# Kernel tuning notes

Hardware: AMD Instinct MI355X
Metric: run time of the kernel (lower is better)

The kernel has to match this reference:

```python
import jax, jax.numpy as jnp
import numpy as np

N_NODES = 50000
N_EDGES = 800000
IN_FEATS = 128
OUT_FEATS = 256
EPS = 1e-5


def _layer_norm(x, g, b):
    mu = jnp.mean(x, axis=-1, keepdims=True)
    var = jnp.var(x, axis=-1, keepdims=True)
    return (x - mu) * jax.lax.rsqrt(var + EPS) * g + b


def setup_inputs() -> dict:
    key = jax.random.key(0)
    ks = jax.random.split(key, 6)
    h = jax.random.normal(ks[0], (N_NODES, IN_FEATS), dtype=jnp.float32)
    src = jax.random.randint(ks[1], (N_EDGES,), 0, N_NODES, dtype=jnp.int32)
    dst = jax.random.randint(ks[2], (N_EDGES,), 0, N_NODES, dtype=jnp.int32)
    s_in = 1.0 / np.sqrt(IN_FEATS)
    s_out = 1.0 / np.sqrt(OUT_FEATS)
    return {
        "h": h,
        "src": src,
        "dst": dst,
        "ln1_g": jnp.ones((IN_FEATS,), jnp.float32),
        "ln1_b": jnp.zeros((IN_FEATS,), jnp.float32),
        "W_self": jax.random.normal(ks[3], (IN_FEATS, OUT_FEATS), jnp.float32) * s_in,
        "W_neigh": jax.random.normal(ks[4], (IN_FEATS, OUT_FEATS), jnp.float32) * s_in,
        "b_neigh": jnp.zeros((OUT_FEATS,), jnp.float32),
        "ln2_g": jnp.ones((OUT_FEATS,), jnp.float32),
        "ln2_b": jnp.zeros((OUT_FEATS,), jnp.float32),
        "W_si": jax.random.normal(ks[5], (OUT_FEATS, OUT_FEATS), jnp.float32) * s_out,
        "b_si": jnp.zeros((OUT_FEATS,), jnp.float32),
    }


def reference(h, src, dst, ln1_g, ln1_b, W_self, W_neigh, b_neigh, ln2_g, ln2_b, W_si, b_si):
    # Pre-norm
    h = _layer_norm(h, ln1_g, ln1_b)
    h_skip = h
    # SAGEConv 'mean': gather src features, segment-mean over dst
    msg = h[src]  # [E, in_feats]
    agg = jax.ops.segment_sum(msg, dst, num_segments=N_NODES)  # [N, in_feats]
    deg = jax.ops.segment_sum(jnp.ones((src.shape[0],), h.dtype), dst, num_segments=N_NODES)
    mean_neigh = agg / jnp.maximum(deg, 1.0)[:, None]
    conv = h @ W_self + mean_neigh @ W_neigh + b_neigh  # [N, out_feats]
    # dropout is identity in eval mode
    # residual skip with channel repeat (out_feat_factor = 2)
    conv = conv + jnp.repeat(h_skip, OUT_FEATS // IN_FEATS, axis=-1)
    # self-interaction: norm -> Linear -> ELU -> residual
    x = _layer_norm(conv, ln2_g, ln2_b)
    out = jax.nn.elu(x @ W_si + b_si) + x
    return out
```

## Files before the change

kernel.cpp:

```cpp
#include <hip/hip_runtime.h>
#include <math.h>

#define N_NODES 50000
#define N_EDGES 800000
#define IN_F 128
#define OUT_F 256
#define EPS 1e-5f
#define BM 16
#define NSCAN 196

typedef __attribute__((ext_vector_type(8))) short short8;
typedef __attribute__((ext_vector_type(4))) float f32x4;

__device__ inline float wave_reduce_sum(float v) {
    #pragma unroll
    for (int m = 32; m >= 1; m >>= 1) v += __shfl_xor(v, m, 64);
    return v;
}

__device__ inline unsigned short f2bf(float f) {
    unsigned int x = __float_as_uint(f);
    return (unsigned short)((x + 0x7fffu + ((x >> 16) & 1u)) >> 16);
}
__device__ inline float bf2f(unsigned short u) {
    return __uint_as_float((unsigned int)u << 16);
}
__device__ inline void split2(float v, unsigned short& hi, unsigned short& lo) {
    hi = f2bf(v);
    lo = f2bf(v - bf2f(hi));
}

__global__ __launch_bounds__(256) void ln1_kernel(const float* __restrict__ h,
        const float* __restrict__ g, const float* __restrict__ b,
        float* __restrict__ hln) {
    int wave = threadIdx.x >> 6;
    int lane = threadIdx.x & 63;
    int row = blockIdx.x * 4 + wave;
    if (row >= N_NODES) return;
    float2 v = ((const float2*)(h + (size_t)row * IN_F))[lane];
    float s  = wave_reduce_sum(v.x + v.y);
    float sq = wave_reduce_sum(v.x * v.x + v.y * v.y);
    float mu = s * (1.0f / IN_F);
    float var = sq * (1.0f / IN_F) - mu * mu;
    float rs = rsqrtf(var + EPS);
    float2 gv = ((const float2*)g)[lane];
    float2 bv = ((const float2*)b)[lane];
    float2 o;
    o.x = (v.x - mu) * rs * gv.x + bv.x;
    o.y = (v.y - mu) * rs * gv.y + bv.y;
    ((float2*)(hln + (size_t)row * IN_F))[lane] = o;
}

__global__ __launch_bounds__(256) void prep_kernel(const float* __restrict__ Wself,
        const float* __restrict__ Wneigh, const float* __restrict__ Wsi,
        unsigned int* __restrict__ W2Th, unsigned int* __restrict__ W2Tl,
        unsigned int* __restrict__ WsiTh, unsigned int* __restrict__ WsiTl) {
    __shared__ float tile[64][65];
    int bx = blockIdx.x;
    int mat = bx >> 4;
    int tr = ((bx >> 2) & 3) * 64;
    int tc = (bx & 3) * 64;
    int t = threadIdx.x;
    int c = t & 63, r0 = t >> 6;
    for (int i = 0; i < 16; ++i) {
        int k = tr + r0 + i * 4;
        float v;
        if (mat == 0) v = (k < 128) ? Wself[(size_t)k * 256 + tc + c]
                                    : Wneigh[(size_t)(k - 128) * 256 + tc + c];
        else          v = Wsi[(size_t)k * 256 + tc + c];
        tile[r0 + i * 4][c] = v;
    }
    __syncthreads();
    unsigned int* oh = (mat == 0) ? W2Th : WsiTh;
    unsigned int* ol = (mat == 0) ? W2Tl : WsiTl;
    int c2 = t & 31, rr = t >> 5;
    for (int i = 0; i < 8; ++i) {
        int n = rr + i * 8;
        float a = tile[c2 * 2][n];
        float b = tile[c2 * 2 + 1][n];
        unsigned short ah, al, bh, bl;
        split2(a, ah, al);
        split2(b, bh, bl);
        size_t idx = (size_t)(tc + n) * 128 + (tr >> 1) + c2;
        oh[idx] = (unsigned int)ah | ((unsigned int)bh << 16);
        ol[idx] = (unsigned int)al | ((unsigned int)bl << 16);
    }
}

__global__ __launch_bounds__(256) void hist_kernel(const int* __restrict__ dst,
                                                   int* __restrict__ cnt) {
    int e = blockIdx.x * 256 + threadIdx.x;
    if (e < N_EDGES) atomicAdd(&cnt[dst[e]], 1);
}

__global__ __launch_bounds__(256) void scan1_kernel(const int* __restrict__ cnt,
        int* __restrict__ curs, int* __restrict__ bsum) {
    int t = threadIdx.x;
    int i = blockIdx.x * 256 + t;
    int v = (i < N_NODES) ? cnt[i] : 0;
    int x = v;
    #pragma unroll
    for (int off = 1; off < 64; off <<= 1) {
        int y = __shfl_up(x, off, 64);
        if ((t & 63) >= off) x += y;
    }
    __shared__ int wsum[4];
    if ((t & 63) == 63) wsum[t >> 6] = x;
    __syncthreads();
    int wofs = 0;
    for (int w = 0; w < (t >> 6); ++w) wofs += wsum[w];
    int incl = x + wofs;
    if (i < N_NODES) curs[i] = incl - v;
    if (t == 255) bsum[blockIdx.x] = incl;
}

__global__ __launch_bounds__(256) void scan2_kernel(int* __restrict__ bsum) {
    int t = threadIdx.x;
    int v = (t < NSCAN) ? bsum[t] : 0;
    int x = v;
    #pragma unroll
    for (int off = 1; off < 64; off <<= 1) {
        int y = __shfl_up(x, off, 64);
        if ((t & 63) >= off) x += y;
    }
    __shared__ int wsum[4];
    if ((t & 63) == 63) wsum[t >> 6] = x;
    __syncthreads();
    int wofs = 0;
    for (int w = 0; w < (t >> 6); ++w) wofs += wsum[w];
    if (t < NSCAN) bsum[t] = x + wofs - v;
}

__global__ __launch_bounds__(256) void scan3_kernel(int* __restrict__ curs,
        const int* __restrict__ bsum) {
    int i = blockIdx.x * 256 + threadIdx.x;
    if (i < N_NODES) curs[i] += bsum[blockIdx.x];
}

__global__ __launch_bounds__(256) void fill_kernel(const int* __restrict__ src,
        const int* __restrict__ dst, int* __restrict__ curs, int* __restrict__ eidx) {
    int e = blockIdx.x * 256 + threadIdx.x;
    if (e >= N_EDGES) return;
    int d = dst[e];
    int pos = atomicAdd(&curs[d], 1);
    eidx[pos] = src[e];
}

__global__ __launch_bounds__(256) void gather_kernel(const float* __restrict__ hln,
        const int* __restrict__ cnt, const int* __restrict__ curs,
        const int* __restrict__ eidx, float* __restrict__ mean) {
    int wave = threadIdx.x >> 6;
    int lane = threadIdx.x & 63;
    int row = blockIdx.x * 4 + wave;
    if (row >= N_NODES) return;
    int deg = cnt[row];
    int end = curs[row];
    int start = end - deg;
    float2 acc = make_float2(0.f, 0.f);
    for (int j0 = 0; j0 < deg; j0 += 64) {
        int mye = (j0 + lane < deg) ? eidx[start + j0 + lane] : 0;
        int m = min(64, deg - j0);
        for (int jj = 0; jj < m; ++jj) {
            int s = __shfl(mye, jj, 64);
            float2 v = ((const float2*)(hln + (size_t)s * IN_F))[lane];
            acc.x += v.x;
            acc.y += v.y;
        }
    }
    float scale = 1.0f / fmaxf((float)deg, 1.0f);
    float2 o; o.x = acc.x * scale; o.y = acc.y * scale;
    ((float2*)(mean + (size_t)row * IN_F))[lane] = o;
}

__global__ __launch_bounds__(256) void fused_kernel(
        const float* __restrict__ hlnf, const float* __restrict__ meanf,
        const unsigned short* __restrict__ W2Th, const unsigned short* __restrict__ W2Tl,
        const unsigned short* __restrict__ WsiTh, const unsigned short* __restrict__ WsiTl,
        const float* __restrict__ bneigh, const float* __restrict__ ln2g,
        const float* __restrict__ ln2b, const float* __restrict__ bsi,
        float* __restrict__ out) {
    __shared__ float sAf[BM][264];
    __shared__ unsigned short sAh[BM][264];
    __shared__ unsigned short sAl[BM][264];
    __shared__ float sC[BM][260];
    __shared__ float spart[4][BM][2];

    const int t = threadIdx.x;
    const int lane = t & 63;
    const int wave = t >> 6;
    const int lrow = lane & 15;
    const int lk = (lane >> 4) * 8;
    const int base = blockIdx.x * BM;

    for (int i = t; i < BM * 64; i += 256) {
        int r = i >> 6, ch = i & 63;
        int node = base + r;
        float4 v = (ch < 32) ? ((const float4*)(hlnf + (size_t)node * IN_F))[ch]
                             : ((const float4*)(meanf + (size_t)node * IN_F))[ch - 32];
        int cb = (ch < 32) ? ch * 4 : 128 + (ch - 32) * 4;
        *(float4*)&sAf[r][cb] = v;
        unsigned short h0, l0, h1, l1, h2, l2, h3, l3;
        split2(v.x, h0, l0); split2(v.y, h1, l1);
        split2(v.z, h2, l2); split2(v.w, h3, l3);
        uint2 ph, pl;
        ph.x = (unsigned int)h0 | ((unsigned int)h1 << 16);
        ph.y = (unsigned int)h2 | ((unsigned int)h3 << 16);
        pl.x = (unsigned int)l0 | ((unsigned int)l1 << 16);
        pl.y = (unsigned int)l2 | ((unsigned int)l3 << 16);
        *(uint2*)&sAh[r][cb] = ph;
        *(uint2*)&sAl[r][cb] = pl;
    }
    __syncthreads();

    f32x4 am[4];
    #pragma unroll
    for (int cf = 0; cf < 4; ++cf) am[cf] = (f32x4)(0.f);
    #pragma unroll
    for (int k0 = 0; k0 < 256; k0 += 32) {
        short8 ah = *(const short8*)&sAh[lrow][k0 + lk];
        short8 al = *(const short8*)&sAl[lrow][k0 + lk];
        #pragma unroll
        for (int cf = 0; cf < 4; ++cf) {
            int col = wave * 64 + cf * 16 + lrow;
            short8 bh = *(const short8*)(W2Th + (size_t)col * 256 + k0 + lk);
            short8 bl = *(const short8*)(W2Tl + (size_t)col * 256 + k0 + lk);
            am[cf] = __builtin_amdgcn_mfma_f32_16x16x32_bf16(ah, bh, am[cf], 0, 0, 0);
            am[cf] = __builtin_amdgcn_mfma_f32_16x16x32_bf16(al, bh, am[cf], 0, 0, 0);
            am[cf] = __builtin_amdgcn_mfma_f32_16x16x32_bf16(ah, bl, am[cf], 0, 0, 0);
        }
    }

    #pragma unroll
    for (int cf = 0; cf < 4; ++cf) {
        int col = wave * 64 + cf * 16 + lrow;
        float bn = bneigh[col];
        #pragma unroll
        for (int q = 0; q < 4; ++q) {
            int row = (lane >> 4) * 4 + q;
            sC[row][col] = am[cf][q] + bn + sAf[row][col >> 1];
        }
    }
    __syncthreads();

    float cv[BM];
    {
        #pragma unroll
        for (int r = 0; r < BM; ++r) {
            float c = sC[r][t];
            cv[r] = c;
            float s  = wave_reduce_sum(c);
            float sq = wave_reduce_sum(c * c);
            if (lane == 0) { spart[wave][r][0] = s; spart[wave][r][1] = sq; }
        }
        __syncthreads();
        float g2 = ln2g[t];
        float b2 = ln2b[t];
        #pragma unroll
        for (int r = 0; r < BM; ++r) {
            float s  = spart[0][r][0] + spart[1][r][0] + spart[2][r][0] + spart[3][r][0];
            float sq = spart[0][r][1] + spart[1][r][1] + spart[2][r][1] + spart[3][r][1];
            float mu = s * (1.0f / OUT_F);
            float var = sq * (1.0f / OUT_F) - mu * mu;
            float rs = rsqrtf(var + EPS);
            float x = (cv[r] - mu) * rs * g2 + b2;
            sC[r][t] = x;
            unsigned short hh, ll;
            split2(x, hh, ll);
            sAh[r][t] = hh;
            sAl[r][t] = ll;
        }
    }
    __syncthreads();

    f32x4 am2[4];
    #pragma unroll
    for (int cf = 0; cf < 4; ++cf) am2[cf] = (f32x4)(0.f);
    #pragma unroll
    for (int k0 = 0; k0 < 256; k0 += 32) {
        short8 ah = *(const short8*)&sAh[lrow][k0 + lk];
        short8 al = *(const short8*)&sAl[lrow][k0 + lk];
        #pragma unroll
        for (int cf = 0; cf < 4; ++cf) {
            int col = wave * 64 + cf * 16 + lrow;
            short8 bh = *(const short8*)(WsiTh + (size_t)col * 256 + k0 + lk);
            short8 bl = *(const short8*)(WsiTl + (size_t)col * 256 + k0 + lk);
            am2[cf] = __builtin_amdgcn_mfma_f32_16x16x32_bf16(ah, bh, am2[cf], 0, 0, 0);
            am2[cf] = __builtin_amdgcn_mfma_f32_16x16x32_bf16(al, bh, am2[cf], 0, 0, 0);
            am2[cf] = __builtin_amdgcn_mfma_f32_16x16x32_bf16(ah, bl, am2[cf], 0, 0, 0);
        }
    }

    #pragma unroll
    for (int cf = 0; cf < 4; ++cf) {
        int col = wave * 64 + cf * 16 + lrow;
        float bs = bsi[col];
        #pragma unroll
        for (int q = 0; q < 4; ++q) {
            int row = (lane >> 4) * 4 + q;
            float x = sC[row][col];
            float z = am2[cf][q] + bs;
            float e = (z > 0.f) ? z : (expf(z) - 1.0f);
            sC[row][col] = e + x;
        }
    }
    __syncthreads();

    for (int i = t; i < BM * 64; i += 256) {
        int r = i >> 6, c4 = i & 63;
        int node = base + r;
        ((float4*)(out + (size_t)node * OUT_F))[c4] = *(const float4*)&sC[r][c4 * 4];
    }
}

extern "C" void kernel_launch(void* const* d_in, const int* in_sizes, int n_in,
                              void* d_out, int out_size, void* d_ws, size_t ws_size,
                              hipStream_t stream) {
    const float* h      = (const float*)d_in[0];
    const int*   src    = (const int*)d_in[1];
    const int*   dst    = (const int*)d_in[2];
    const float* ln1g   = (const float*)d_in[3];
    const float* ln1b   = (const float*)d_in[4];
    const float* Wself  = (const float*)d_in[5];
    const float* Wneigh = (const float*)d_in[6];
    const float* bneigh = (const float*)d_in[7];
    const float* ln2g   = (const float*)d_in[8];
    const float* ln2b   = (const float*)d_in[9];
    const float* Wsi    = (const float*)d_in[10];
    const float* bsi    = (const float*)d_in[11];
    float* out = (float*)d_out;

    char* ws = (char*)d_ws;
    float* hlnf  = (float*)(ws);
    float* meanf = (float*)(ws + 25600000);
    int* cnt  = (int*)(ws + 51200000);
    int* curs = (int*)(ws + 51400064);
    int* eidx = (int*)(ws + 51600064);
    int* bsum = (int*)(ws + 54800064);
    unsigned short* W2Th  = (unsigned short*)(ws + 54800896);
    unsigned short* W2Tl  = (unsigned short*)(ws + 54931968);
    unsigned short* WsiTh = (unsigned short*)(ws + 55063040);
    unsigned short* WsiTl = (unsigned short*)(ws + 55194112);

    hipMemsetAsync(cnt, 0, 200000, stream);

    prep_kernel<<<32, 256, 0, stream>>>(Wself, Wneigh, Wsi,
                                        (unsigned int*)W2Th, (unsigned int*)W2Tl,
                                        (unsigned int*)WsiTh, (unsigned int*)WsiTl);
    ln1_kernel<<<N_NODES / 4, 256, 0, stream>>>(h, ln1g, ln1b, hlnf);
    hist_kernel<<<N_EDGES / 256, 256, 0, stream>>>(dst, cnt);
    scan1_kernel<<<NSCAN, 256, 0, stream>>>(cnt, curs, bsum);
    scan2_kernel<<<1, 256, 0, stream>>>(bsum);
    scan3_kernel<<<NSCAN, 256, 0, stream>>>(curs, bsum);
    fill_kernel<<<N_EDGES / 256, 256, 0, stream>>>(src, dst, curs, eidx);
    gather_kernel<<<N_NODES / 4, 256, 0, stream>>>(hlnf, cnt, curs, eidx, meanf);
    fused_kernel<<<N_NODES / BM, 256, 0, stream>>>(hlnf, meanf,
                                                   W2Th, W2Tl, WsiTh, WsiTl,
                                                   bneigh, ln2g, ln2b, bsi, out);
}
```

Baseline: 470.4 us.

## Store LN1 and mean outputs as bf16 hi/lo split, widen fused tile to 32 rows

LN1 and the gather now write pre-split bf16 hi/lo pairs into one shared [N,256] A buffer, so the fused kernel reads MFMA operands straight from global memory instead of loading floats and splitting them in LDS. The gather still reads the same number of bytes per neighbour (two 4-byte words), but it must reconstruct the float from the pair. The fused kernel now handles 32 rows per block, computes LN2 statistics from registers with a partial-shuffle reduction instead of a staging buffer, and writes output directly from registers. The cost is less coalesced direct global stores, plus bounds clamps for a partial last tile.

```diff
diff --git a/kernel.cpp b/kernel.cpp
--- a/kernel.cpp
+++ b/kernel.cpp
@@ -6,7 +6,7 @@
 #define IN_F 128
 #define OUT_F 256
 #define EPS 1e-5f
-#define BM 16
+#define BMF 32
 #define NSCAN 196
 
 typedef __attribute__((ext_vector_type(8))) short short8;
@@ -25,6 +25,8 @@
 __device__ inline float bf2f(unsigned short u) {
     return __uint_as_float((unsigned int)u << 16);
 }
+__device__ inline float bflo(unsigned int u) { return __uint_as_float(u << 16); }
+__device__ inline float bfhi(unsigned int u) { return __uint_as_float(u & 0xffff0000u); }
 __device__ inline void split2(float v, unsigned short& hi, unsigned short& lo) {
     hi = f2bf(v);
     lo = f2bf(v - bf2f(hi));
@@ -32,7 +34,7 @@
 
 __global__ __launch_bounds__(256) void ln1_kernel(const float* __restrict__ h,
         const float* __restrict__ g, const float* __restrict__ b,
-        float* __restrict__ hln) {
+        unsigned short* __restrict__ Ahi, unsigned short* __restrict__ Alo) {
     int wave = threadIdx.x >> 6;
     int lane = threadIdx.x & 63;
     int row = blockIdx.x * 4 + wave;
@@ -45,10 +47,13 @@
     float rs = rsqrtf(var + EPS);
     float2 gv = ((const float2*)g)[lane];
     float2 bv = ((const float2*)b)[lane];
-    float2 o;
-    o.x = (v.x - mu) * rs * gv.x + bv.x;
-    o.y = (v.y - mu) * rs * gv.y + bv.y;
-    ((float2*)(hln + (size_t)row * IN_F))[lane] = o;
+    float ox = (v.x - mu) * rs * gv.x + bv.x;
+    float oy = (v.y - mu) * rs * gv.y + bv.y;
+    unsigned short hx, lx, hy, ly;
+    split2(ox, hx, lx);
+    split2(oy, hy, ly);
+    ((unsigned int*)Ahi)[(size_t)row * 128 + lane] = (unsigned int)hx | ((unsigned int)hy << 16);
+    ((unsigned int*)Alo)[(size_t)row * 128 + lane] = (unsigned int)lx | ((unsigned int)ly << 16);
 }
 
 __global__ __launch_bounds__(256) void prep_kernel(const float* __restrict__ Wself,
@@ -146,9 +151,10 @@
     eidx[pos] = src[e];
 }
 
-__global__ __launch_bounds__(256) void gather_kernel(const float* __restrict__ hln,
+__global__ __launch_bounds__(256) void gather_kernel(
+        unsigned short* __restrict__ Ahi, unsigned short* __restrict__ Alo,
         const int* __restrict__ cnt, const int* __restrict__ curs,
-        const int* __restrict__ eidx, float* __restrict__ mean) {
+        const int* __restrict__ eidx) {
     int wave = threadIdx.x >> 6;
     int lane = threadIdx.x & 63;
     int row = blockIdx.x * 4 + wave;
@@ -162,153 +168,201 @@
         int m = min(64, deg - j0);
         for (int jj = 0; jj < m; ++jj) {
             int s = __shfl(mye, jj, 64);
-            float2 v = ((const float2*)(hln + (size_t)s * IN_F))[lane];
-            acc.x += v.x;
-            acc.y += v.y;
-        }
-    }
-    float scale = 1.0f / fmaxf((float)deg, 1.0f);
-    float2 o; o.x = acc.x * scale; o.y = acc.y * scale;
-    ((float2*)(mean + (size_t)row * IN_F))[lane] = o;
-}
-
-__global__ __launch_bounds__(256) void fused_kernel(
-        const float* __restrict__ hlnf, const float* __restrict__ meanf,
+            unsigned int uh = ((const unsigned int*)Ahi)[(size_t)s * 128 + lane];
+            unsigned int ul = ((const unsigned int*)Alo)[(size_t)s * 128 + lane];
+            acc.x += bflo(uh) + bflo(ul);
+            acc.y += bfhi(uh) + bfhi(ul);
+        }
+    }
+    float sc = 1.0f / fmaxf((float)deg, 1.0f);
+    float mx = acc.x * sc, my = acc.y * sc;
+    unsigned short hx, lx, hy, ly;
+    split2(mx, hx, lx);
+    split2(my, hy, ly);
+    ((unsigned int*)Ahi)[(size_t)row * 128 + 64 + lane] = (unsigned int)hx | ((unsigned int)hy << 16);
+    ((unsigned int*)Alo)[(size_t)row * 128 + 64 + lane] = (unsigned int)lx | ((unsigned int)ly << 16);
+}
+
+__global__ __launch_bounds__(256, 3) void fused_kernel(
+        const unsigned short* __restrict__ Ahi, const unsigned short* __restrict__ Alo,
         const unsigned short* __restrict__ W2Th, const unsigned short* __restrict__ W2Tl,
         const unsigned short* __restrict__ WsiTh, const unsigned short* __restrict__ WsiTl,
         const float* __restrict__ bneigh, const float* __restrict__ ln2g,
         const float* __restrict__ ln2b, const float* __restrict__ bsi,
         float* __restrict__ out) {
-    __shared__ float sAf[BM][264];
-    __shared__ unsigned short sAh[BM][264];
-    __shared__ unsigned short sAl[BM][264];
-    __shared__ float sC[BM][260];
-    __shared__ float spart[4][BM][2];
+    __shared__ unsigned short sxh[BMF][270];
+    __shared__ unsigned short sxl[BMF][270];
+    __shared__ unsigned short sHh[BMF][132];
+    __shared__ unsigned short sHl[BMF][132];
+    __shared__ float spart[4][BMF][2];
 
     const int t = threadIdx.x;
     const int lane = t & 63;
     const int wave = t >> 6;
     const int lrow = lane & 15;
-    const int lk = (lane >> 4) * 8;
-    const int base = blockIdx.x * BM;
-
-    for (int i = t; i < BM * 64; i += 256) {
-        int r = i >> 6, ch = i & 63;
-        int node = base + r;
-        float4 v = (ch < 32) ? ((const float4*)(hlnf + (size_t)node * IN_F))[ch]
-                             : ((const float4*)(meanf + (size_t)node * IN_F))[ch - 32];
-        int cb = (ch < 32) ? ch * 4 : 128 + (ch - 32) * 4;
-        *(float4*)&sAf[r][cb] = v;
-        unsigned short h0, l0, h1, l1, h2, l2, h3, l3;
-        split2(v.x, h0, l0); split2(v.y, h1, l1);
-        split2(v.z, h2, l2); split2(v.w, h3, l3);
-        uint2 ph, pl;
-        ph.x = (unsigned int)h0 | ((unsigned int)h1 << 16);
-        ph.y = (unsigned int)h2 | ((unsigned int)h3 << 16);
-        pl.x = (unsigned int)l0 | ((unsigned int)l1 << 16);
-        pl.y = (unsigned int)l2 | ((unsigned int)l3 << 16);
-        *(uint2*)&sAh[r][cb] = ph;
-        *(uint2*)&sAl[r][cb] = pl;
-    }
-    __syncthreads();
-
-    f32x4 am[4];
-    #pragma unroll
-    for (int cf = 0; cf < 4; ++cf) am[cf] = (f32x4)(0.f);
+    const int khalf = lane >> 4;
+    const int lk = khalf * 8;
+    const int base = blockIdx.x * BMF;
+    const int cbase = wave * 64;
+
+    #pragma unroll
+    for (int i = 0; i < 2; ++i) {
+        int idx = t + i * 256;
+        int r = idx >> 4;
+        int c8 = (idx & 15) * 8;
+        int nd = min(base + r, N_NODES - 1);
+        *(uint4*)&sHh[r][c8] = *(const uint4*)&Ahi[(size_t)nd * 256 + c8];
+        *(uint4*)&sHl[r][c8] = *(const uint4*)&Alo[(size_t)nd * 256 + c8];
+    }
+
+    const int ar0 = min(base + lrow, N_NODES - 1);
+    const int ar1 = min(base + 16 + lrow, N_NODES - 1);
+    const unsigned short* a0ph = Ahi + (size_t)ar0 * 256;
+    const unsigned short* a0pl = Alo + (size_t)ar0 * 256;
+    const unsigned short* a1ph = Ahi + (size_t)ar1 * 256;
+    const unsigned short* a1pl = Alo + (size_t)ar1 * 256;
+
+    f32x4 am[2][4];
+    #pragma unroll
+    for (int rf = 0; rf < 2; ++rf)
+        #pragma unroll
+        for (int cf = 0; cf < 4; ++cf) am[rf][cf] = (f32x4)(0.f);
+
     #pragma unroll
     for (int k0 = 0; k0 < 256; k0 += 32) {
-        short8 ah = *(const short8*)&sAh[lrow][k0 + lk];
-        short8 al = *(const short8*)&sAl[lrow][k0 + lk];
+        short8 a0h = *(const short8*)&a0ph[k0 + lk];
+        short8 a0l = *(const short8*)&a0pl[k0 + lk];
+        short8 a1h = *(const short8*)&a1ph[k0 + lk];
+        short8 a1l = *(const short8*)&a1pl[k0 + lk];
         #pragma unroll
         for (int cf = 0; cf < 4; ++cf) {
-            int col = wave * 64 + cf * 16 + lrow;
+            int col = cbase + cf * 16 + lrow;
             short8 bh = *(const short8*)(W2Th + (size_t)col * 256 + k0 + lk);
             short8 bl = *(const short8*)(W2Tl + (size_t)col * 256 + k0 + lk);
-            am[cf] = __builtin_amdgcn_mfma_f32_16x16x32_bf16(ah, bh, am[cf], 0, 0, 0);
-            am[cf] = __builtin_amdgcn_mfma_f32_16x16x32_bf16(al, bh, am[cf], 0, 0, 0);
-            am[cf] = __builtin_amdgcn_mfma_f32_16x16x32_bf16(ah, bl, am[cf], 0, 0, 0);
-        }
-    }
-
+            am[0][cf] = __builtin_amdgcn_mfma_f32_16x16x32_bf16(a0h, bh, am[0][cf], 0, 0, 0);
+            am[0][cf] = __builtin_amdgcn_mfma_f32_16x16x32_bf16(a0l, bh, am[0][cf], 0, 0, 0);
+            am[0][cf] = __builtin_amdgcn_mfma_f32_16x16x32_bf16(a0h, bl, am[0][cf], 0, 0, 0);
+            am[1][cf] = __builtin_amdgcn_mfma_f32_16x16x32_bf16(a1h, bh, am[1][cf], 0, 0, 0);
+            am[1][cf] = __builtin_amdgcn_mfma_f32_16x16x32_bf16(a1l, bh, am[1][cf], 0, 0, 0);
+            am[1][cf] = __builtin_amdgcn_mfma_f32_16x16x32_bf16(a1h, bl, am[1][cf], 0, 0, 0);
+        }
+    }
+    __syncthreads();
+
+    float bn[4], g2[4], b2[4];
     #pragma unroll
     for (int cf = 0; cf < 4; ++cf) {
-        int col = wave * 64 + cf * 16 + lrow;
-        float bn = bneigh[col];
+        int col = cbase + cf * 16 + lrow;
+        bn[cf] = bneigh[col];
+        g2[cf] = ln2g[col];
+        b2[cf] = ln2b[col];
+    }
+    #pragma unroll
+    for (int rf = 0; rf < 2; ++rf)
+        #pragma unroll
+        for (int cf = 0; cf < 4; ++cf) {
+            int hc = (cbase + cf * 16 + lrow) >> 1;
+            #pragma unroll
+            for (int q = 0; q < 4; ++q) {
+                int row = rf * 16 + khalf * 4 + q;
+                float skip = bf2f(sHh[row][hc]) + bf2f(sHl[row][hc]);
+                am[rf][cf][q] += bn[cf] + skip;
+            }
+        }
+
+    #pragma unroll
+    for (int rf = 0; rf < 2; ++rf)
         #pragma unroll
         for (int q = 0; q < 4; ++q) {
-            int row = (lane >> 4) * 4 + q;
-            sC[row][col] = am[cf][q] + bn + sAf[row][col >> 1];
-        }
-    }
-    __syncthreads();
-
-    float cv[BM];
-    {
-        #pragma unroll
-        for (int r = 0; r < BM; ++r) {
-            float c = sC[r][t];
-            cv[r] = c;
-            float s  = wave_reduce_sum(c);
-            float sq = wave_reduce_sum(c * c);
-            if (lane == 0) { spart[wave][r][0] = s; spart[wave][r][1] = sq; }
-        }
-        __syncthreads();
-        float g2 = ln2g[t];
-        float b2 = ln2b[t];
-        #pragma unroll
-        for (int r = 0; r < BM; ++r) {
-            float s  = spart[0][r][0] + spart[1][r][0] + spart[2][r][0] + spart[3][r][0];
-            float sq = spart[0][r][1] + spart[1][r][1] + spart[2][r][1] + spart[3][r][1];
-            float mu = s * (1.0f / OUT_F);
-            float var = sq * (1.0f / OUT_F) - mu * mu;
-            float rs = rsqrtf(var + EPS);
-            float x = (cv[r] - mu) * rs * g2 + b2;
-            sC[r][t] = x;
-            unsigned short hh, ll;
-            split2(x, hh, ll);
-            sAh[r][t] = hh;
-            sAl[r][t] = ll;
-        }
-    }
-    __syncthreads();
-
-    f32x4 am2[4];
-    #pragma unroll
-    for (int cf = 0; cf < 4; ++cf) am2[cf] = (f32x4)(0.f);
+            float s  = am[rf][0][q] + am[rf][1][q] + am[rf][2][q] + am[rf][3][q];
+            float sq = am[rf][0][q] * am[rf][0][q] + am[rf][1][q] * am[rf][1][q]
+                     + am[rf][2][q] * am[rf][2][q] + am[rf][3][q] * am[rf][3][q];
+            #pragma unroll
+            for (int m = 1; m <= 8; m <<= 1) {
+                s  += __shfl_xor(s, m, 64);
+                sq += __shfl_xor(sq, m, 64);
+            }
+            if (lrow == 0) {
+                int row = rf * 16 + khalf * 4 + q;
+                spart[wave][row][0] = s;
+                spart[wave][row][1] = sq;
+            }
+        }
+    __syncthreads();
+
+    float mu[2][4], rsv[2][4];
+    #pragma unroll
+    for (int rf = 0; rf < 2; ++rf)
+        #pragma unroll
+        for (int q = 0; q < 4; ++q) {
+            int row = rf * 16 + khalf * 4 + q;
+            float s  = spart[0][row][0] + spart[1][row][0] + spart[2][row][0] + spart[3][row][0];
+            float sq = spart[0][row][1] + spart[1][row][1] + spart[2][row][1] + spart[3][row][1];
+            float m_ = s * (1.0f / OUT_F);
+            float v_ = sq * (1.0f / OUT_F) - m_ * m_;
+            mu[rf][q]  = m_;
+            rsv[rf][q] = rsqrtf(v_ + EPS);
+        }
+    #pragma unroll
+    for (int rf = 0; rf < 2; ++rf)
+        #pragma unroll
+        for (int cf = 0; cf < 4; ++cf) {
+            int col = cbase + cf * 16 + lrow;
+            #pragma unroll
+            for (int q = 0; q < 4; ++q) {
+                int row = rf * 16 + khalf * 4 + q;
+                float x = (am[rf][cf][q] - mu[rf][q]) * rsv[rf][q] * g2[cf] + b2[cf];
+                am[rf][cf][q] = x;
+                unsigned short hh, ll;
+                split2(x, hh, ll);
+                sxh[row][col] = hh;
+                sxl[row][col] = ll;
+            }
+        }
+    __syncthreads();
+
+    f32x4 am2[2][4];
+    #pragma unroll
+    for (int rf = 0; rf < 2; ++rf)
+        #pragma unroll
+        for (int cf = 0; cf < 4; ++cf) am2[rf][cf] = (f32x4)(0.f);
+
     #pragma unroll
     for (int k0 = 0; k0 < 256; k0 += 32) {
-        short8 ah = *(const short8*)&sAh[lrow][k0 + lk];
-        short8 al = *(const short8*)&sAl[lrow][k0 + lk];
+        short8 x0h = *(const short8*)&sxh[lrow][k0 + lk];
+        short8 x0l = *(const short8*)&sxl[lrow][k0 + lk];
+        short8 x1h = *(const short8*)&sxh[16 + lrow][k0 + lk];
+        short8 x1l = *(const short8*)&sxl[16 + lrow][k0 + lk];
         #pragma unroll
         for (int cf = 0; cf < 4; ++cf) {
-            int col = wave * 64 + cf * 16 + lrow;
+            int col = cbase + cf * 16 + lrow;
             short8 bh = *(const short8*)(WsiTh + (size_t)col * 256 + k0 + lk);
             short8 bl = *(const short8*)(WsiTl + (size_t)col * 256 + k0 + lk);
-            am2[cf] = __builtin_amdgcn_mfma_f32_16x16x32_bf16(ah, bh, am2[cf], 0, 0, 0);
-            am2[cf] = __builtin_amdgcn_mfma_f32_16x16x32_bf16(al, bh, am2[cf], 0, 0, 0);
-            am2[cf] = __builtin_amdgcn_mfma_f32_16x16x32_bf16(ah, bl, am2[cf], 0, 0, 0);
+            am2[0][cf] = __builtin_amdgcn_mfma_f32_16x16x32_bf16(x0h, bh, am2[0][cf], 0, 0, 0);
+            am2[0][cf] = __builtin_amdgcn_mfma_f32_16x16x32_bf16(x0l, bh, am2[0][cf], 0, 0, 0);
+            am2[0][cf] = __builtin_amdgcn_mfma_f32_16x16x32_bf16(x0h, bl, am2[0][cf], 0, 0, 0);
+            am2[1][cf] = __builtin_amdgcn_mfma_f32_16x16x32_bf16(x1h, bh, am2[1][cf], 0, 0, 0);
+            am2[1][cf] = __builtin_amdgcn_mfma_f32_16x16x32_bf16(x1l, bh, am2[1][cf], 0, 0, 0);
+            am2[1][cf] = __builtin_amdgcn_mfma_f32_16x16x32_bf16(x1h, bl, am2[1][cf], 0, 0, 0);
         }
     }
 
     #pragma unroll
     for (int cf = 0; cf < 4; ++cf) {
-        int col = wave * 64 + cf * 16 + lrow;
+        int col = cbase + cf * 16 + lrow;
         float bs = bsi[col];
         #pragma unroll
-        for (int q = 0; q < 4; ++q) {
-            int row = (lane >> 4) * 4 + q;
-            float x = sC[row][col];
-            float z = am2[cf][q] + bs;
-            float e = (z > 0.f) ? z : (expf(z) - 1.0f);
-            sC[row][col] = e + x;
-        }
-    }
-    __syncthreads();
-
-    for (int i = t; i < BM * 64; i += 256) {
-        int r = i >> 6, c4 = i & 63;
-        int node = base + r;
-        ((float4*)(out + (size_t)node * OUT_F))[c4] = *(const float4*)&sC[r][c4 * 4];
+        for (int rf = 0; rf < 2; ++rf)
+            #pragma unroll
+            for (int q = 0; q < 4; ++q) {
+                int row = rf * 16 + khalf * 4 + q;
+                int node = base + row;
+                if (node < N_NODES) {
+                    float z = am2[rf][cf][q] + bs;
+                    float e = (z > 0.f) ? z : (expf(z) - 1.0f);
+                    out[(size_t)node * OUT_F + col] = e + am[rf][cf][q];
+                }
+            }
     }
 }
 
@@ -330,8 +384,8 @@
     float* out = (float*)d_out;
 
     char* ws = (char*)d_ws;
-    float* hlnf  = (float*)(ws);
-    float* meanf = (float*)(ws + 25600000);
+    unsigned short* Ahi = (unsigned short*)(ws);
+    unsigned short* Alo = (unsigned short*)(ws + 25600000);
     int* cnt  = (int*)(ws + 51200000);
     int* curs = (int*)(ws + 51400064);
     int* eidx = (int*)(ws + 51600064);
@@ -346,14 +400,14 @@
     prep_kernel<<<32, 256, 0, stream>>>(Wself, Wneigh, Wsi,
                                         (unsigned int*)W2Th, (unsigned int*)W2Tl,
                                         (unsigned int*)WsiTh, (unsigned int*)WsiTl);
-    ln1_kernel<<<N_NODES / 4, 256, 0, stream>>>(h, ln1g, ln1b, hlnf);
+    ln1_kernel<<<N_NODES / 4, 256, 0, stream>>>(h, ln1g, ln1b, Ahi, Alo);
     hist_kernel<<<N_EDGES / 256, 256, 0, stream>>>(dst, cnt);
     scan1_kernel<<<NSCAN, 256, 0, stream>>>(cnt, curs, bsum);
     scan2_kernel<<<1, 256, 0, stream>>>(bsum);
     scan3_kernel<<<NSCAN, 256, 0, stream>>>(curs, bsum);
     fill_kernel<<<N_EDGES / 256, 256, 0, stream>>>(src, dst, curs, eidx);
-    gather_kernel<<<N_NODES / 4, 256, 0, stream>>>(hlnf, cnt, curs, eidx, meanf);
-    fused_kernel<<<N_NODES / BM, 256, 0, stream>>>(hlnf, meanf,
+    gather_kernel<<<N_NODES / 4, 256, 0, stream>>>(Ahi, Alo, cnt, curs, eidx);
+    fused_kernel<<<(N_NODES + BMF - 1) / BMF, 256, 0, stream>>>(Ahi, Alo,
                                                    W2Th, W2Tl, WsiTh, WsiTl,
                                                    bneigh, ln2g, ln2b, bsi, out);
 }
```

Result: faster. 406.5 us (-13.6%).
